# Performance work log

Hardware: AMD Instinct MI355X
Metric: run time of the kernel (lower is better)

## Reference

```python
import jax, jax.numpy as jnp
import numpy as np
import math

N_HEADS = 16
DIM = 1024
HEAD_DIM = DIM // N_HEADS
BS, QLEN = 4, 2048


def setup_inputs() -> dict:
    key = jax.random.key(0)
    ks = jax.random.split(key, 10)
    s = 0.02
    return {
        "input": jax.random.normal(ks[0], (BS, QLEN, DIM), dtype=jnp.float32),
        "mask": jnp.ones((BS, QLEN), dtype=jnp.int32),
        "wq": jax.random.normal(ks[1], (DIM, DIM), dtype=jnp.float32) * s,
        "bq": jax.random.normal(ks[2], (DIM,), dtype=jnp.float32) * s,
        "wk": jax.random.normal(ks[3], (DIM, DIM), dtype=jnp.float32) * s,
        "bk": jax.random.normal(ks[4], (DIM,), dtype=jnp.float32) * s,
        "wv": jax.random.normal(ks[5], (DIM, DIM), dtype=jnp.float32) * s,
        "bv": jax.random.normal(ks[6], (DIM,), dtype=jnp.float32) * s,
        "wo": jax.random.normal(ks[7], (DIM, DIM), dtype=jnp.float32) * s,
        "bo": jax.random.normal(ks[8], (DIM,), dtype=jnp.float32) * s,
    }


def reference(input, mask, wq, bq, wk, bk, wv, bv, wo, bo):
    bs, qlen, dim = input.shape
    # torch Linear: y = x @ W.T + b
    def proj(x, w, b):
        y = jnp.einsum("bsd,ed->bse", x, w) + b
        # [bs, seq, n_heads, head_dim] -> [bs, n_heads, seq, head_dim]
        return y.reshape(bs, qlen, N_HEADS, HEAD_DIM).transpose(0, 2, 1, 3)

    q = proj(input, wq, bq) / math.sqrt(HEAD_DIM)
    k = proj(input, wk, bk)
    v = proj(input, wv, bv)

    # scores: [bs, n_heads, qlen, klen]
    scores = jnp.einsum("bhqd,bhkd->bhqk", q, k)
    pad = (mask == 0)[:, None, None, :]  # (bs,1,1,klen)
    scores = jnp.where(pad, -jnp.inf, scores)
    weights = jax.nn.softmax(scores.astype(jnp.float32), axis=-1).astype(scores.dtype)
    # dropout p=0 (eval mode) -> identity
    context = jnp.einsum("bhqk,bhkd->bhqd", weights, v)
    context = context.transpose(0, 2, 1, 3).reshape(bs, qlen, dim)
    out = jnp.einsum("bsd,ed->bse", context, wo) + bo
    return out
```

## Files before the change

kernel.cpp:

```cpp
#include <hip/hip_runtime.h>
#include <cstdint>

typedef unsigned int u32;
typedef unsigned short u16;
typedef __attribute__((ext_vector_type(4))) short bf16x4;
typedef __attribute__((ext_vector_type(8))) short bf16x8;
typedef __attribute__((ext_vector_type(4))) float f32x4;

#define QSCALE 0.1803368801111204f

typedef const void __attribute__((address_space(1)))* gas1p;
typedef void __attribute__((address_space(3)))* las3p;

__device__ __forceinline__ void gload_lds16(const void* g, void* l) {
  __builtin_amdgcn_global_load_lds((gas1p)g, (las3p)l, 16, 0, 0);
}

#if __has_builtin(__builtin_amdgcn_exp2f)
#define EXP2F(x) __builtin_amdgcn_exp2f(x)
#else
#define EXP2F(x) exp2f(x)
#endif

__device__ __forceinline__ u16 f2bf(float f) {
  __bf16 h = (__bf16)f;
  return __builtin_bit_cast(u16, h);
}

__global__ void cvt_kernel(const float* __restrict__ src, u16* __restrict__ dst, int n4) {
  int i = blockIdx.x * blockDim.x + threadIdx.x;
  int stride = gridDim.x * blockDim.x;
  for (; i < n4; i += stride) {
    float4 f = ((const float4*)src)[i];
    ushort4 o;
    o.x = f2bf(f.x); o.y = f2bf(f.y); o.z = f2bf(f.z); o.w = f2bf(f.w);
    ((ushort4*)dst)[i] = o;
  }
}

__global__ void maskflag_kernel(const int* __restrict__ mask, int* __restrict__ flags) {
  int id = blockIdx.x * blockDim.x + threadIdx.x;
  if (id < 128) {
    int b = id >> 5, ch = id & 31;
    const int4* p = (const int4*)(mask + b * 2048 + ch * 64);
    int ok = 1;
#pragma unroll
    for (int j = 0; j < 16; j++) {
      int4 v = p[j];
      ok &= (v.x != 0) & (v.y != 0) & (v.z != 0) & (v.w != 0);
    }
    flags[id] = ok;
  }
}

__global__ __launch_bounds__(256, 2)
void gemm_qkv(const u16* __restrict__ X,
              const u16* __restrict__ Wq, const u16* __restrict__ Wk, const u16* __restrict__ Wv,
              const float* __restrict__ bq, const float* __restrict__ bk, const float* __restrict__ bv,
              u16* __restrict__ Qh, u16* __restrict__ Kh, u16* __restrict__ Vt) {
  __shared__ u16 smem[16384];
  const int t = threadIdx.x;
  const int lane = t & 63;
  const int wid = t >> 6;
  const int g = lane >> 4, q16 = lane & 15;
  const int wr = wid >> 1, wc = wid & 1;
  const int n0 = blockIdx.x * 128;
  const int m0 = blockIdx.y * 128;
  const int z = blockIdx.z;
  const u16* B = (z == 0) ? Wq : (z == 1) ? Wk : Wv;
  const float* bias = (z == 0) ? bq : (z == 1) ? bk : bv;

  auto stage = [&](int buf, int k0) {
#pragma unroll
    for (int i = 0; i < 2; i++) {
      int idx = i * 256 + t;
      int row = idx >> 2, sl = idx & 3;
      int ss = sl ^ ((row >> 1) & 3);
      gload_lds16(X + (size_t)(m0 + row) * 1024 + k0 + ss * 8, (char*)(smem + buf * 4096) + idx * 16);
      gload_lds16(B + (size_t)(n0 + row) * 1024 + k0 + ss * 8, (char*)(smem + 8192 + buf * 4096) + idx * 16);
    }
  };

  f32x4 acc[4][4] = {};
  stage(0, 0);
  __syncthreads();
  for (int kt = 0; kt < 32; kt++) {
    if (kt < 31) stage((kt + 1) & 1, (kt + 1) * 32);
    const u16* Ab = smem + (kt & 1) * 4096;
    const u16* Bb = smem + 8192 + (kt & 1) * 4096;
    bf16x8 af[4], bfr[4];
#pragma unroll
    for (int mi = 0; mi < 4; mi++) {
      int row = wr * 64 + mi * 16 + q16;
      int ps = g ^ ((row >> 1) & 3);
      af[mi] = *(const bf16x8*)((const char*)Ab + row * 64 + ps * 16);
      int rowb = wc * 64 + mi * 16 + q16;
      int psb = g ^ ((rowb >> 1) & 3);
      bfr[mi] = *(const bf16x8*)((const char*)Bb + rowb * 64 + psb * 16);
    }
#pragma unroll
    for (int mi = 0; mi < 4; mi++)
#pragma unroll
      for (int ni = 0; ni < 4; ni++)
        acc[mi][ni] = __builtin_amdgcn_mfma_f32_16x16x32_bf16(af[mi], bfr[ni], acc[mi][ni], 0, 0, 0);
    __syncthreads();
  }

  if (z == 2) {
    u16* T = smem;
    const int TP = 132;
#pragma unroll 1
    for (int half = 0; half < 2; half++) {
      __syncthreads();
      if (wc == half) {
#pragma unroll
        for (int ni = 0; ni < 4; ni++) {
          int dloc = ni * 16 + q16;
          float bv_ = bias[n0 + half * 64 + dloc];
#pragma unroll
          for (int mi = 0; mi < 4; mi++) {
            ushort4 o;
            o.x = f2bf(acc[mi][ni][0] + bv_);
            o.y = f2bf(acc[mi][ni][1] + bv_);
            o.z = f2bf(acc[mi][ni][2] + bv_);
            o.w = f2bf(acc[mi][ni][3] + bv_);
            *(ushort4*)&T[dloc * TP + wr * 64 + mi * 16 + g * 4] = o;
          }
        }
      }
      __syncthreads();
      {
        int dloc = t >> 2, c = t & 3;
        int h = (n0 >> 6) + half;
        int b = m0 >> 11;
        size_t gbase = ((size_t)(b * 16 + h) * 64 + dloc) * 2048 + (m0 & 2047) + c * 32;
#pragma unroll
        for (int j = 0; j < 8; j++) {
          ushort4 v = *(const ushort4*)&T[dloc * TP + c * 32 + j * 4];
          *(ushort4*)&Vt[gbase + j * 4] = v;
        }
      }
    }
    return;
  }

#pragma unroll
  for (int ni = 0; ni < 4; ni++) {
    int col = n0 + wc * 64 + ni * 16 + q16;
    float bv_ = bias[col];
    int h = col >> 6, d = col & 63;
#pragma unroll
    for (int mi = 0; mi < 4; mi++) {
#pragma unroll
      for (int r = 0; r < 4; r++) {
        int row = m0 + wr * 64 + mi * 16 + g * 4 + r;
        int b = row >> 11, sq = row & 2047;
        float v = acc[mi][ni][r] + bv_;
        if (z == 0) {
          Qh[(((size_t)(b * 16 + h)) * 2048 + sq) * 64 + d] = f2bf(v * QSCALE);
        } else {
          Kh[(((size_t)(b * 16 + h)) * 2048 + sq) * 64 + d] = f2bf(v);
        }
      }
    }
  }
}

__global__ __launch_bounds__(256, 2)
void gemm_out(const u16* __restrict__ X, const u16* __restrict__ W,
              const float* __restrict__ bias, float* __restrict__ Out) {
  __shared__ u16 As[2][128 * 32];
  __shared__ u16 Bs[2][128 * 32];
  const int t = threadIdx.x;
  const int lane = t & 63;
  const int wid = t >> 6;
  const int g = lane >> 4, q16 = lane & 15;
  const int wr = wid >> 1, wc = wid & 1;
  const int n0 = blockIdx.x * 128;
  const int m0 = blockIdx.y * 128;

  auto stage = [&](int buf, int k0) {
#pragma unroll
    for (int i = 0; i < 2; i++) {
      int idx = i * 256 + t;
      int row = idx >> 2, sl = idx & 3;
      int ss = sl ^ ((row >> 1) & 3);
      gload_lds16(X + (size_t)(m0 + row) * 1024 + k0 + ss * 8, (char*)&As[buf][0] + idx * 16);
      gload_lds16(W + (size_t)(n0 + row) * 1024 + k0 + ss * 8, (char*)&Bs[buf][0] + idx * 16);
    }
  };

  f32x4 acc[4][4] = {};
  stage(0, 0);
  __syncthreads();
  for (int kt = 0; kt < 32; kt++) {
    if (kt < 31) stage((kt + 1) & 1, (kt + 1) * 32);
    const u16* Ab = &As[kt & 1][0];
    const u16* Bb = &Bs[kt & 1][0];
    bf16x8 af[4], bfr[4];
#pragma unroll
    for (int mi = 0; mi < 4; mi++) {
      int row = wr * 64 + mi * 16 + q16;
      int ps = g ^ ((row >> 1) & 3);
      af[mi] = *(const bf16x8*)((const char*)Ab + row * 64 + ps * 16);
      int rowb = wc * 64 + mi * 16 + q16;
      int psb = g ^ ((rowb >> 1) & 3);
      bfr[mi] = *(const bf16x8*)((const char*)Bb + rowb * 64 + psb * 16);
    }
#pragma unroll
    for (int mi = 0; mi < 4; mi++)
#pragma unroll
      for (int ni = 0; ni < 4; ni++)
        acc[mi][ni] = __builtin_amdgcn_mfma_f32_16x16x32_bf16(af[mi], bfr[ni], acc[mi][ni], 0, 0, 0);
    __syncthreads();
  }

#pragma unroll
  for (int ni = 0; ni < 4; ni++) {
    int col = n0 + wc * 64 + ni * 16 + q16;
    float bv_ = bias[col];
#pragma unroll
    for (int mi = 0; mi < 4; mi++) {
#pragma unroll
      for (int r = 0; r < 4; r++) {
        int row = m0 + wr * 64 + mi * 16 + g * 4 + r;
        Out[(size_t)row * 1024 + col] = acc[mi][ni][r] + bv_;
      }
    }
  }
}

__global__ __launch_bounds__(256, 4)
void attn_kernel(const u16* __restrict__ Qh, const u16* __restrict__ Kh,
                 const u16* __restrict__ Vt, const int* __restrict__ mask,
                 const int* __restrict__ mflags, u16* __restrict__ ctx) {
  __shared__ u16 Ks[2][64 * 64];
  __shared__ u16 Vs[2][64 * 64];
  const int t = threadIdx.x;
  const int lane = t & 63;
  const int w = t >> 6;
  const int g = lane >> 4, q16 = lane & 15;
  const int flat = blockIdx.y * 32 + blockIdx.x;
  const int xcd = flat & 7, slot = flat >> 3;
  const int bh = xcd + 8 * (slot >> 5);
  const int qb = slot & 31;
  const int b = bh >> 4, h = bh & 15;

  bf16x8 qf[2];
  {
    const u16* qp = Qh + ((size_t)bh * 2048 + qb * 64 + w * 16 + q16) * 64;
    qf[0] = *(const bf16x8*)(qp + g * 8);
    qf[1] = *(const bf16x8*)(qp + 32 + g * 8);
  }

  auto stage = [&](int buf, int kv0) {
#pragma unroll
    for (int i = 0; i < 2; i++) {
      int idx = i * 256 + t;
      int row = idx >> 3, sl = idx & 7;
      int ss = sl ^ (row & 7);
      gload_lds16(Kh + ((size_t)bh * 2048 + kv0 + row) * 64 + ss * 8, (char*)&Ks[buf][0] + idx * 16);
      gload_lds16(Vt + ((size_t)bh * 64 + row) * 2048 + kv0 + ss * 8, (char*)&Vs[buf][0] + idx * 16);
    }
  };

  f32x4 oacc[4] = {};
  float lsum = 0.f;
  const int4* mrow = (const int4*)(mask + b * 2048);
  const int* mf = mflags + b * 32;

  stage(0, 0);
  __syncthreads();

  for (int it = 0; it < 32; it++) {
    const int kv0 = it * 64;
    if (it < 31) stage((it + 1) & 1, kv0 + 64);
    const u16* Kb = &Ks[it & 1][0];
    const u16* Vb = &Vs[it & 1][0];

    f32x4 sac[4] = {};
#pragma unroll
    for (int ks = 0; ks < 2; ks++) {
#pragma unroll
      for (int mb = 0; mb < 4; mb++) {
        int row = mb * 16 + q16;
        int ps = (ks * 4 + g) ^ (row & 7);
        bf16x8 kf = *(const bf16x8*)((const char*)Kb + row * 128 + ps * 16);
        sac[mb] = __builtin_amdgcn_mfma_f32_16x16x32_bf16(kf, qf[ks], sac[mb], 0, 0, 0);
      }
    }

    float p[16];
    if (mf[it]) {
#pragma unroll
      for (int mb = 0; mb < 4; mb++) {
        p[mb * 4 + 0] = EXP2F(sac[mb][0]);
        p[mb * 4 + 1] = EXP2F(sac[mb][1]);
        p[mb * 4 + 2] = EXP2F(sac[mb][2]);
        p[mb * 4 + 3] = EXP2F(sac[mb][3]);
      }
    } else {
#pragma unroll
      for (int mb = 0; mb < 4; mb++) {
        int4 mv = mrow[(kv0 + mb * 16 + g * 4) >> 2];
        p[mb * 4 + 0] = mv.x ? EXP2F(sac[mb][0]) : 0.f;
        p[mb * 4 + 1] = mv.y ? EXP2F(sac[mb][1]) : 0.f;
        p[mb * 4 + 2] = mv.z ? EXP2F(sac[mb][2]) : 0.f;
        p[mb * 4 + 3] = mv.w ? EXP2F(sac[mb][3]) : 0.f;
      }
    }
#pragma unroll
    for (int j = 0; j < 16; j++) lsum += p[j];

#pragma unroll
    for (int ks = 0; ks < 2; ks++) {
      bf16x8 pf;
#pragma unroll
      for (int j = 0; j < 8; j++) pf[j] = (short)f2bf(p[8 * ks + j]);
#pragma unroll
      for (int nb = 0; nb < 4; nb++) {
        int row = nb * 16 + q16;
        int c0 = 8 * ks + g;
        int c1 = 8 * ks + 4 + g;
        int a0 = row * 128 + (((c0 >> 1) ^ (row & 7)) << 4) + ((c0 & 1) << 3);
        int a1 = row * 128 + (((c1 >> 1) ^ (row & 7)) << 4) + ((c1 & 1) << 3);
        bf16x4 vA = *(const bf16x4*)((const char*)Vb + a0);
        bf16x4 vB = *(const bf16x4*)((const char*)Vb + a1);
        bf16x8 vf = __builtin_shufflevector(vA, vB, 0, 1, 2, 3, 4, 5, 6, 7);
        oacc[nb] = __builtin_amdgcn_mfma_f32_16x16x32_bf16(pf, vf, oacc[nb], 0, 0, 0);
      }
    }
    __syncthreads();
  }

  lsum += __shfl_xor(lsum, 16);
  lsum += __shfl_xor(lsum, 32);
  float rinv = (lsum > 0.f) ? 1.f / lsum : 0.f;
  float r0 = __shfl(rinv, (g << 4) + g * 4 + 0);
  float r1 = __shfl(rinv, (g << 4) + g * 4 + 1);
  float r2 = __shfl(rinv, (g << 4) + g * 4 + 2);
  float r3 = __shfl(rinv, (g << 4) + g * 4 + 3);
#pragma unroll
  for (int nb = 0; nb < 4; nb++) {
    int col = h * 64 + nb * 16 + q16;
    size_t base = ((size_t)b * 2048 + qb * 64 + w * 16 + g * 4) * 1024 + col;
    ctx[base + (size_t)0 * 1024] = f2bf(oacc[nb][0] * r0);
    ctx[base + (size_t)1 * 1024] = f2bf(oacc[nb][1] * r1);
    ctx[base + (size_t)2 * 1024] = f2bf(oacc[nb][2] * r2);
    ctx[base + (size_t)3 * 1024] = f2bf(oacc[nb][3] * r3);
  }
}

extern "C" void kernel_launch(void* const* d_in, const int* in_sizes, int n_in,
                              void* d_out, int out_size, void* d_ws, size_t ws_size,
                              hipStream_t stream) {
  (void)in_sizes; (void)n_in; (void)out_size; (void)ws_size;
  const float* input = (const float*)d_in[0];
  const int* mask = (const int*)d_in[1];
  const float* wq = (const float*)d_in[2];
  const float* bq = (const float*)d_in[3];
  const float* wk = (const float*)d_in[4];
  const float* bk = (const float*)d_in[5];
  const float* wv = (const float*)d_in[6];
  const float* bv = (const float*)d_in[7];
  const float* wo = (const float*)d_in[8];
  const float* bo = (const float*)d_in[9];
  float* out = (float*)d_out;

  u16* xb = (u16*)d_ws;
  u16* wqb = xb + (size_t)8192 * 1024;
  u16* wkb = wqb + (size_t)1024 * 1024;
  u16* wvb = wkb + (size_t)1024 * 1024;
  u16* wob = wvb + (size_t)1024 * 1024;
  u16* Qh = wob + (size_t)1024 * 1024;
  u16* Kh = Qh + (size_t)64 * 2048 * 64;
  u16* Vt = Kh + (size_t)64 * 2048 * 64;
  int* mflags = (int*)(Vt + (size_t)64 * 64 * 2048);
  u16* ctx = xb;

  cvt_kernel<<<2048, 256, 0, stream>>>(input, xb, 8192 * 1024 / 4);
  cvt_kernel<<<1024, 256, 0, stream>>>(wq, wqb, 1024 * 1024 / 4);
  cvt_kernel<<<1024, 256, 0, stream>>>(wk, wkb, 1024 * 1024 / 4);
  cvt_kernel<<<1024, 256, 0, stream>>>(wv, wvb, 1024 * 1024 / 4);
  cvt_kernel<<<1024, 256, 0, stream>>>(wo, wob, 1024 * 1024 / 4);
  maskflag_kernel<<<1, 128, 0, stream>>>(mask, mflags);

  gemm_qkv<<<dim3(8, 64, 3), 256, 0, stream>>>(xb, wqb, wkb, wvb, bq, bk, bv, Qh, Kh, Vt);
  attn_kernel<<<dim3(32, 64), 256, 0, stream>>>(Qh, Kh, Vt, mask, mflags, ctx);
  gemm_out<<<dim3(8, 64), 256, 0, stream>>>(ctx, wob, bo, out);
}
```

Measured before the change: 310.0 us.

## Double attention query tile per wave and pre-permute V for single LDS reads

Each attention wave now handles 32 query rows instead of 16, so every K and V fragment read from LDS feeds two MFMAs, and the grid is halved. The QKV GEMM epilogue writes V in a permuted column order, which lets the PV loop use one 16-byte swizzled LDS load instead of two 8-byte loads plus a shuffle. The four weight-conversion launches are also merged into one kernel. Register pressure rises (double accumulators and score arrays) under launch_bounds(256,4), and having fewer blocks may reduce latency hiding.

```diff
diff --git a/kernel.cpp b/kernel.cpp
--- a/kernel.cpp
+++ b/kernel.cpp
@@ -3,7 +3,6 @@
 
 typedef unsigned int u32;
 typedef unsigned short u16;
-typedef __attribute__((ext_vector_type(4))) short bf16x4;
 typedef __attribute__((ext_vector_type(8))) short bf16x8;
 typedef __attribute__((ext_vector_type(4))) float f32x4;
 
@@ -38,6 +37,27 @@
   }
 }
 
+__global__ void cvt4_kernel(const float* __restrict__ s0, const float* __restrict__ s1,
+                            const float* __restrict__ s2, const float* __restrict__ s3,
+                            u16* __restrict__ d0, u16* __restrict__ d1,
+                            u16* __restrict__ d2, u16* __restrict__ d3, int n4) {
+  const float* s; u16* d;
+  switch (blockIdx.y) {
+    case 0: s = s0; d = d0; break;
+    case 1: s = s1; d = d1; break;
+    case 2: s = s2; d = d2; break;
+    default: s = s3; d = d3; break;
+  }
+  int i = blockIdx.x * blockDim.x + threadIdx.x;
+  int stride = gridDim.x * blockDim.x;
+  for (; i < n4; i += stride) {
+    float4 f = ((const float4*)s)[i];
+    ushort4 o;
+    o.x = f2bf(f.x); o.y = f2bf(f.y); o.z = f2bf(f.z); o.w = f2bf(f.w);
+    ((ushort4*)d)[i] = o;
+  }
+}
+
 __global__ void maskflag_kernel(const int* __restrict__ mask, int* __restrict__ flags) {
   int id = blockIdx.x * blockDim.x + threadIdx.x;
   if (id < 128) {
@@ -57,7 +77,7 @@
 void gemm_qkv(const u16* __restrict__ X,
               const u16* __restrict__ Wq, const u16* __restrict__ Wk, const u16* __restrict__ Wv,
               const float* __restrict__ bq, const float* __restrict__ bk, const float* __restrict__ bv,
-              u16* __restrict__ Qh, u16* __restrict__ Kh, u16* __restrict__ Vt) {
+              u16* __restrict__ Qh, u16* __restrict__ Kh, u16* __restrict__ Vp) {
   __shared__ u16 smem[16384];
   const int t = threadIdx.x;
   const int lane = t & 63;
@@ -133,11 +153,12 @@
         int dloc = t >> 2, c = t & 3;
         int h = (n0 >> 6) + half;
         int b = m0 >> 11;
-        size_t gbase = ((size_t)(b * 16 + h) * 64 + dloc) * 2048 + (m0 & 2047) + c * 32;
+        size_t gbase = ((size_t)(b * 16 + h) * 64 + dloc) * 2048 + (m0 & 2047)
+                     + (c >> 1) * 64 + (c & 1) * 32;
 #pragma unroll
         for (int j = 0; j < 8; j++) {
           ushort4 v = *(const ushort4*)&T[dloc * TP + c * 32 + j * 4];
-          *(ushort4*)&Vt[gbase + j * 4] = v;
+          *(ushort4*)&Vp[gbase + (j & 3) * 8 + (j >> 2) * 4] = v;
         }
       }
     }
@@ -232,7 +253,7 @@
 
 __global__ __launch_bounds__(256, 4)
 void attn_kernel(const u16* __restrict__ Qh, const u16* __restrict__ Kh,
-                 const u16* __restrict__ Vt, const int* __restrict__ mask,
+                 const u16* __restrict__ Vp, const int* __restrict__ mask,
                  const int* __restrict__ mflags, u16* __restrict__ ctx) {
   __shared__ u16 Ks[2][64 * 64];
   __shared__ u16 Vs[2][64 * 64];
@@ -240,17 +261,18 @@
   const int lane = t & 63;
   const int w = t >> 6;
   const int g = lane >> 4, q16 = lane & 15;
-  const int flat = blockIdx.y * 32 + blockIdx.x;
+  const int flat = blockIdx.y * 16 + blockIdx.x;
   const int xcd = flat & 7, slot = flat >> 3;
-  const int bh = xcd + 8 * (slot >> 5);
-  const int qb = slot & 31;
+  const int bh = xcd + 8 * (slot >> 4);
+  const int qb = slot & 15;
   const int b = bh >> 4, h = bh & 15;
 
-  bf16x8 qf[2];
-  {
-    const u16* qp = Qh + ((size_t)bh * 2048 + qb * 64 + w * 16 + q16) * 64;
-    qf[0] = *(const bf16x8*)(qp + g * 8);
-    qf[1] = *(const bf16x8*)(qp + 32 + g * 8);
+  bf16x8 qf[2][2];
+#pragma unroll
+  for (int qg = 0; qg < 2; qg++) {
+    const u16* qp = Qh + ((size_t)bh * 2048 + qb * 128 + w * 32 + qg * 16 + q16) * 64;
+    qf[qg][0] = *(const bf16x8*)(qp + g * 8);
+    qf[qg][1] = *(const bf16x8*)(qp + 32 + g * 8);
   }
 
   auto stage = [&](int buf, int kv0) {
@@ -260,12 +282,12 @@
       int row = idx >> 3, sl = idx & 7;
       int ss = sl ^ (row & 7);
       gload_lds16(Kh + ((size_t)bh * 2048 + kv0 + row) * 64 + ss * 8, (char*)&Ks[buf][0] + idx * 16);
-      gload_lds16(Vt + ((size_t)bh * 64 + row) * 2048 + kv0 + ss * 8, (char*)&Vs[buf][0] + idx * 16);
+      gload_lds16(Vp + ((size_t)bh * 64 + row) * 2048 + kv0 + ss * 8, (char*)&Vs[buf][0] + idx * 16);
     }
   };
 
-  f32x4 oacc[4] = {};
-  float lsum = 0.f;
+  f32x4 oacc[2][4] = {};
+  float lsum[2] = {0.f, 0.f};
   const int4* mrow = (const int4*)(mask + b * 2048);
   const int* mf = mflags + b * 32;
 
@@ -278,7 +300,7 @@
     const u16* Kb = &Ks[it & 1][0];
     const u16* Vb = &Vs[it & 1][0];
 
-    f32x4 sac[4] = {};
+    f32x4 sac[2][4] = {};
 #pragma unroll
     for (int ks = 0; ks < 2; ks++) {
 #pragma unroll
@@ -286,68 +308,77 @@
         int row = mb * 16 + q16;
         int ps = (ks * 4 + g) ^ (row & 7);
         bf16x8 kf = *(const bf16x8*)((const char*)Kb + row * 128 + ps * 16);
-        sac[mb] = __builtin_amdgcn_mfma_f32_16x16x32_bf16(kf, qf[ks], sac[mb], 0, 0, 0);
-      }
-    }
-
-    float p[16];
-    if (mf[it]) {
-#pragma unroll
-      for (int mb = 0; mb < 4; mb++) {
-        p[mb * 4 + 0] = EXP2F(sac[mb][0]);
-        p[mb * 4 + 1] = EXP2F(sac[mb][1]);
-        p[mb * 4 + 2] = EXP2F(sac[mb][2]);
-        p[mb * 4 + 3] = EXP2F(sac[mb][3]);
-      }
-    } else {
-#pragma unroll
-      for (int mb = 0; mb < 4; mb++) {
-        int4 mv = mrow[(kv0 + mb * 16 + g * 4) >> 2];
-        p[mb * 4 + 0] = mv.x ? EXP2F(sac[mb][0]) : 0.f;
-        p[mb * 4 + 1] = mv.y ? EXP2F(sac[mb][1]) : 0.f;
-        p[mb * 4 + 2] = mv.z ? EXP2F(sac[mb][2]) : 0.f;
-        p[mb * 4 + 3] = mv.w ? EXP2F(sac[mb][3]) : 0.f;
-      }
-    }
-#pragma unroll
-    for (int j = 0; j < 16; j++) lsum += p[j];
+        sac[0][mb] = __builtin_amdgcn_mfma_f32_16x16x32_bf16(kf, qf[0][ks], sac[0][mb], 0, 0, 0);
+        sac[1][mb] = __builtin_amdgcn_mfma_f32_16x16x32_bf16(kf, qf[1][ks], sac[1][mb], 0, 0, 0);
+      }
+    }
+
+    const int mfit = mf[it];
+    bf16x8 pf[2][2];
+#pragma unroll
+    for (int qg = 0; qg < 2; qg++) {
+      float p[16];
+      if (mfit) {
+#pragma unroll
+        for (int mb = 0; mb < 4; mb++) {
+          p[mb * 4 + 0] = EXP2F(sac[qg][mb][0]);
+          p[mb * 4 + 1] = EXP2F(sac[qg][mb][1]);
+          p[mb * 4 + 2] = EXP2F(sac[qg][mb][2]);
+          p[mb * 4 + 3] = EXP2F(sac[qg][mb][3]);
+        }
+      } else {
+#pragma unroll
+        for (int mb = 0; mb < 4; mb++) {
+          int4 mv = mrow[(kv0 + mb * 16 + g * 4) >> 2];
+          p[mb * 4 + 0] = mv.x ? EXP2F(sac[qg][mb][0]) : 0.f;
+          p[mb * 4 + 1] = mv.y ? EXP2F(sac[qg][mb][1]) : 0.f;
+          p[mb * 4 + 2] = mv.z ? EXP2F(sac[qg][mb][2]) : 0.f;
+          p[mb * 4 + 3] = mv.w ? EXP2F(sac[qg][mb][3]) : 0.f;
+        }
+      }
+      float ps_ = 0.f;
+#pragma unroll
+      for (int j = 0; j < 16; j++) ps_ += p[j];
+      lsum[qg] += ps_;
+#pragma unroll
+      for (int ks = 0; ks < 2; ks++)
+#pragma unroll
+        for (int j = 0; j < 8; j++) pf[qg][ks][j] = (short)f2bf(p[8 * ks + j]);
+    }
 
 #pragma unroll
     for (int ks = 0; ks < 2; ks++) {
-      bf16x8 pf;
-#pragma unroll
-      for (int j = 0; j < 8; j++) pf[j] = (short)f2bf(p[8 * ks + j]);
 #pragma unroll
       for (int nb = 0; nb < 4; nb++) {
         int row = nb * 16 + q16;
-        int c0 = 8 * ks + g;
-        int c1 = 8 * ks + 4 + g;
-        int a0 = row * 128 + (((c0 >> 1) ^ (row & 7)) << 4) + ((c0 & 1) << 3);
-        int a1 = row * 128 + (((c1 >> 1) ^ (row & 7)) << 4) + ((c1 & 1) << 3);
-        bf16x4 vA = *(const bf16x4*)((const char*)Vb + a0);
-        bf16x4 vB = *(const bf16x4*)((const char*)Vb + a1);
-        bf16x8 vf = __builtin_shufflevector(vA, vB, 0, 1, 2, 3, 4, 5, 6, 7);
-        oacc[nb] = __builtin_amdgcn_mfma_f32_16x16x32_bf16(pf, vf, oacc[nb], 0, 0, 0);
+        int ps = (ks * 4 + g) ^ (row & 7);
+        bf16x8 vf = *(const bf16x8*)((const char*)Vb + row * 128 + ps * 16);
+        oacc[0][nb] = __builtin_amdgcn_mfma_f32_16x16x32_bf16(pf[0][ks], vf, oacc[0][nb], 0, 0, 0);
+        oacc[1][nb] = __builtin_amdgcn_mfma_f32_16x16x32_bf16(pf[1][ks], vf, oacc[1][nb], 0, 0, 0);
       }
     }
     __syncthreads();
   }
 
-  lsum += __shfl_xor(lsum, 16);
-  lsum += __shfl_xor(lsum, 32);
-  float rinv = (lsum > 0.f) ? 1.f / lsum : 0.f;
-  float r0 = __shfl(rinv, (g << 4) + g * 4 + 0);
-  float r1 = __shfl(rinv, (g << 4) + g * 4 + 1);
-  float r2 = __shfl(rinv, (g << 4) + g * 4 + 2);
-  float r3 = __shfl(rinv, (g << 4) + g * 4 + 3);
-#pragma unroll
-  for (int nb = 0; nb < 4; nb++) {
-    int col = h * 64 + nb * 16 + q16;
-    size_t base = ((size_t)b * 2048 + qb * 64 + w * 16 + g * 4) * 1024 + col;
-    ctx[base + (size_t)0 * 1024] = f2bf(oacc[nb][0] * r0);
-    ctx[base + (size_t)1 * 1024] = f2bf(oacc[nb][1] * r1);
-    ctx[base + (size_t)2 * 1024] = f2bf(oacc[nb][2] * r2);
-    ctx[base + (size_t)3 * 1024] = f2bf(oacc[nb][3] * r3);
+#pragma unroll
+  for (int qg = 0; qg < 2; qg++) {
+    float ls = lsum[qg];
+    ls += __shfl_xor(ls, 16);
+    ls += __shfl_xor(ls, 32);
+    float rinv = (ls > 0.f) ? 1.f / ls : 0.f;
+    float r0 = __shfl(rinv, (g << 4) + g * 4 + 0);
+    float r1 = __shfl(rinv, (g << 4) + g * 4 + 1);
+    float r2 = __shfl(rinv, (g << 4) + g * 4 + 2);
+    float r3 = __shfl(rinv, (g << 4) + g * 4 + 3);
+#pragma unroll
+    for (int nb = 0; nb < 4; nb++) {
+      int col = h * 64 + nb * 16 + q16;
+      size_t base = ((size_t)b * 2048 + qb * 128 + w * 32 + qg * 16 + g * 4) * 1024 + col;
+      ctx[base + (size_t)0 * 1024] = f2bf(oacc[qg][nb][0] * r0);
+      ctx[base + (size_t)1 * 1024] = f2bf(oacc[qg][nb][1] * r1);
+      ctx[base + (size_t)2 * 1024] = f2bf(oacc[qg][nb][2] * r2);
+      ctx[base + (size_t)3 * 1024] = f2bf(oacc[qg][nb][3] * r3);
+    }
   }
 }
 
@@ -374,18 +405,16 @@
   u16* wob = wvb + (size_t)1024 * 1024;
   u16* Qh = wob + (size_t)1024 * 1024;
   u16* Kh = Qh + (size_t)64 * 2048 * 64;
-  u16* Vt = Kh + (size_t)64 * 2048 * 64;
-  int* mflags = (int*)(Vt + (size_t)64 * 64 * 2048);
+  u16* Vp = Kh + (size_t)64 * 2048 * 64;
+  int* mflags = (int*)(Vp + (size_t)64 * 64 * 2048);
   u16* ctx = xb;
 
   cvt_kernel<<<2048, 256, 0, stream>>>(input, xb, 8192 * 1024 / 4);
-  cvt_kernel<<<1024, 256, 0, stream>>>(wq, wqb, 1024 * 1024 / 4);
-  cvt_kernel<<<1024, 256, 0, stream>>>(wk, wkb, 1024 * 1024 / 4);
-  cvt_kernel<<<1024, 256, 0, stream>>>(wv, wvb, 1024 * 1024 / 4);
-  cvt_kernel<<<1024, 256, 0, stream>>>(wo, wob, 1024 * 1024 / 4);
+  cvt4_kernel<<<dim3(256, 4), 256, 0, stream>>>(wq, wk, wv, wo, wqb, wkb, wvb, wob,
+                                                1024 * 1024 / 4);
   maskflag_kernel<<<1, 128, 0, stream>>>(mask, mflags);
 
-  gemm_qkv<<<dim3(8, 64, 3), 256, 0, stream>>>(xb, wqb, wkb, wvb, bq, bk, bv, Qh, Kh, Vt);
-  attn_kernel<<<dim3(32, 64), 256, 0, stream>>>(Qh, Kh, Vt, mask, mflags, ctx);
+  gemm_qkv<<<dim3(8, 64, 3), 256, 0, stream>>>(xb, wqb, wkb, wvb, bq, bk, bv, Qh, Kh, Vp);
+  attn_kernel<<<dim3(16, 64), 256, 0, stream>>>(Qh, Kh, Vp, mask, mflags, ctx);
   gemm_out<<<dim3(8, 64), 256, 0, stream>>>(ctx, wob, bo, out);
 }
```

After: 284.4 us. 8.3% less time.
